# Kernel tuning notes

Hardware: AMD Instinct MI355X
Metric: run time of the kernel (lower is better)

Reference implementation:

```python
import jax, jax.numpy as jnp
import numpy as np

N = 100_000      # nodes
M = 200_000      # hyperedges
E = 1_000_000    # incidence pairs
D_IN = 64
HEADS, D_OUT = 8, 16   # linear out = 8*16 = 128


def setup_inputs() -> dict:
    key = jax.random.key(0)
    k = jax.random.split(key, 7)
    X = jax.random.normal(k[0], (N, D_IN), dtype=jnp.float32)
    vertex = jax.random.randint(k[1], (E,), 0, N, dtype=jnp.int32)
    edges = jax.random.randint(k[2], (E,), 0, M, dtype=jnp.int32)
    dege = jax.random.uniform(k[3], (M, 1), dtype=jnp.float32)
    degv = jax.random.uniform(k[4], (N, 1), dtype=jnp.float32)
    W = jax.random.normal(k[5], (D_IN, HEADS * D_OUT), dtype=jnp.float32) / np.sqrt(D_IN)
    b = jax.random.normal(k[6], (HEADS * D_OUT,), dtype=jnp.float32) * 0.01
    return {"X": X, "vertex": vertex, "edges": edges, "dege": dege, "degv": degv, "W": W, "b": b}


def reference(X, vertex, edges, dege, degv, W, b):
    n_nodes = X.shape[0]
    n_edges = dege.shape[0]
    # vertex -> hyperedge aggregation (first_aggregate = 'mean')
    Xve = X[vertex]                                               # [E, D]
    sums = jax.ops.segment_sum(Xve, edges, num_segments=n_edges)  # [M, D]
    counts = jax.ops.segment_sum(jnp.ones((edges.shape[0],), X.dtype), edges, num_segments=n_edges)
    Xe = sums / jnp.maximum(counts, 1.0)[:, None]                 # empty edges -> 0
    Xe = Xe * dege
    # hyperedge -> vertex aggregation (sum)
    Xev = Xe[edges]                                               # [E, D]
    Xv = jax.ops.segment_sum(Xev, vertex, num_segments=n_nodes)   # [N, D]
    Xv = Xv * degv
    # normalize_l2: row norm is computed on a DETACHED tensor in torch
    rownorm = jnp.linalg.norm(jax.lax.stop_gradient(Xv), axis=1, keepdims=True)
    scale = jnp.where(rownorm > 0, 1.0 / rownorm, 0.0)
    Xn = Xv * scale
    return Xn @ W + b
```

## Files before the change

kernel.cpp:

```cpp
#include <hip/hip_runtime.h>


#define DIN 64
#define DOUT 128
#define CH 4096
#define BSHIFT 9
#define FINE 512
#define PAYBITS 18
#define PAYMASK ((1u << PAYBITS) - 1u)
#define XB 256

typedef float f32x4 __attribute__((ext_vector_type(4)));
typedef short bf16x8 __attribute__((ext_vector_type(8)));

__device__ __forceinline__ unsigned short f2b(float f) {
  unsigned u = __float_as_uint(f);
  u = u + 0x7fffu + ((u >> 16) & 1u);
  return (unsigned short)(u >> 16);
}
__device__ __forceinline__ float b2f(unsigned s) {
  return __uint_as_float(s << 16);
}

__global__ __launch_bounds__(256) void k_p1(
    const int* __restrict__ vertex, const int* __restrict__ edges,
    int* __restrict__ G, const float* __restrict__ X,
    unsigned short* __restrict__ Xb, int* __restrict__ done,
    int E, int BKE, int BK, int NCH, int total4) {
  if (blockIdx.x == 0 && threadIdx.x == 0) *done = 0;
  if (blockIdx.x >= (unsigned)NCH) {
    int xb = blockIdx.x - NCH;
    for (int i = xb * 256 + threadIdx.x; i < total4; i += XB * 256) {
      float4 a = ((const float4*)X)[i];
      ushort4 r;
      r.x = f2b(a.x); r.y = f2b(a.y); r.z = f2b(a.z); r.w = f2b(a.w);
      ((ushort4*)Xb)[i] = r;
    }
    return;
  }
  __shared__ int h[1024];
  for (int i = threadIdx.x; i < BK; i += 256) h[i] = 0;
  __syncthreads();
  int c = blockIdx.x;
  int s = c * CH, e_ = min(E, s + CH);
  for (int i = s + threadIdx.x; i < e_; i += 256) {
    atomicAdd(&h[edges[i] >> BSHIFT], 1);
    atomicAdd(&h[BKE + (vertex[i] >> BSHIFT)], 1);
  }
  __syncthreads();
  for (int b = threadIdx.x; b < BK; b += 256) G[(size_t)b * NCH + c] = h[b];
}

__global__ __launch_bounds__(256) void k_p1b(
    int* __restrict__ G, int* __restrict__ rowTot, int* __restrict__ bucketBase,
    int* __restrict__ done, int NCH, int BK) {
  int b = blockIdx.x;
  int* row = G + (size_t)b * NCH;
  __shared__ int wsum[4];
  __shared__ int carry;
  __shared__ bool amLast;
  if (threadIdx.x == 0) carry = 0;
  __syncthreads();
  for (int base = 0; base < NCH; base += 256) {
    int i = base + threadIdx.x;
    int v = (i < NCH) ? row[i] : 0;
    int lane = threadIdx.x & 63, wid = threadIdx.x >> 6;
    int inc = v;
    #pragma unroll
    for (int o = 1; o < 64; o <<= 1) {
      int t = __shfl_up(inc, o);
      if (lane >= o) inc += t;
    }
    if (lane == 63) wsum[wid] = inc;
    __syncthreads();
    int woff = carry;
    for (int w = 0; w < wid; ++w) woff += wsum[w];
    int excl = woff + inc - v;
    if (i < NCH) row[i] = excl;
    __syncthreads();
    if (threadIdx.x == 0) carry += wsum[0] + wsum[1] + wsum[2] + wsum[3];
    __syncthreads();
  }
  if (threadIdx.x == 0) {
    rowTot[b] = carry;
    __threadfence();
    amLast = (atomicAdd(done, 1) == gridDim.x - 1);
  }
  __syncthreads();
  if (!amLast) return;

  if (threadIdx.x == 0) carry = 0;
  __syncthreads();
  for (int base = 0; base < BK; base += 256) {
    int i = base + threadIdx.x;
    int v = (i < BK) ? atomicAdd(&rowTot[i], 0) : 0;
    int lane = threadIdx.x & 63, wid = threadIdx.x >> 6;
    int inc = v;
    #pragma unroll
    for (int o = 1; o < 64; o <<= 1) {
      int t = __shfl_up(inc, o);
      if (lane >= o) inc += t;
    }
    if (lane == 63) wsum[wid] = inc;
    __syncthreads();
    int woff = carry;
    for (int w = 0; w < wid; ++w) woff += wsum[w];
    int excl = woff + inc - v;
    if (i < BK) bucketBase[i] = excl;
    __syncthreads();
    if (threadIdx.x == 0) carry += wsum[0] + wsum[1] + wsum[2] + wsum[3];
    __syncthreads();
  }
  if (threadIdx.x == 0) bucketBase[BK] = carry;
}

__global__ __launch_bounds__(256) void p2_scatter(
    const int* __restrict__ vertex, const int* __restrict__ edges,
    const int* __restrict__ G, const int* __restrict__ bucketBase,
    unsigned* __restrict__ temp, int E, int BKE, int BK, int NCH) {
  __shared__ int curs[1024];
  int c = blockIdx.x;
  for (int b = threadIdx.x; b < BK; b += 256)
    curs[b] = bucketBase[b] + G[(size_t)b * NCH + c];
  __syncthreads();
  int s = c * CH, e_ = min(E, s + CH);
  for (int i = s + threadIdx.x; i < e_; i += 256) {
    int e = edges[i], v = vertex[i];
    int pE = atomicAdd(&curs[e >> BSHIFT], 1);
    temp[pE] = ((unsigned)(e & (FINE - 1)) << PAYBITS) | (unsigned)v;
    int pV = atomicAdd(&curs[BKE + (v >> BSHIFT)], 1);
    temp[pV] = ((unsigned)(v & (FINE - 1)) << PAYBITS) | (unsigned)e;
  }
}

__global__ __launch_bounds__(256) void p3_sort(
    const unsigned* __restrict__ temp, const int* __restrict__ bucketBase,
    int* __restrict__ off, int* __restrict__ perm, int BKE, int M, int N) {
  __shared__ int hist[FINE];
  __shared__ int pos[FINE];
  __shared__ int wsum[4];
  int g = blockIdx.x;
  bool isE = g < BKE;
  int gg = isE ? g : g - BKE;
  int keyBase = gg << BSHIFT;
  int cap = isE ? M : N;
  int offBase = (isE ? 0 : M) + keyBase;
  int fineCount = min(FINE, cap - keyBase);
  int pairBase = bucketBase[g], pairEnd = bucketBase[g + 1];
  int cnt = pairEnd - pairBase;

  for (int i = threadIdx.x; i < FINE; i += 256) hist[i] = 0;
  __syncthreads();
  for (int i = threadIdx.x; i < cnt; i += 256)
    atomicAdd(&hist[temp[pairBase + i] >> PAYBITS], 1);
  __syncthreads();

  int t2 = threadIdx.x * 2;
  int a0 = hist[t2], a1 = hist[t2 + 1];
  int tsum = a0 + a1;
  int lane = threadIdx.x & 63, wid = threadIdx.x >> 6;
  int inc = tsum;
  #pragma unroll
  for (int o = 1; o < 64; o <<= 1) {
    int t = __shfl_up(inc, o);
    if (lane >= o) inc += t;
  }
  if (lane == 63) wsum[wid] = inc;
  __syncthreads();
  int woff = 0;
  for (int w = 0; w < wid; ++w) woff += wsum[w];
  int excl = woff + inc - tsum;
  pos[t2] = excl; pos[t2 + 1] = excl + a0;
  __syncthreads();

  for (int f = threadIdx.x; f < fineCount; f += 256)
    off[offBase + f] = pairBase + pos[f] + hist[f];
  for (int f = threadIdx.x; f < FINE; f += 256) pos[f] += pairBase;
  __syncthreads();

  for (int i = threadIdx.x; i < cnt; i += 256) {
    unsigned p = temp[pairBase + i];
    int q = atomicAdd(&pos[p >> PAYBITS], 1);
    perm[q] = (int)(p & PAYMASK);
  }
}


__global__ __launch_bounds__(256) void k_edge(
    const unsigned short* __restrict__ Xb, const int* __restrict__ off,
    const int* __restrict__ perm, const float* __restrict__ dege,
    unsigned short* __restrict__ Xe, int M) {
  long long gid = (long long)blockIdx.x * 256 + threadIdx.x;
  int wv = (int)(gid >> 6);
  int lane = threadIdx.x & 63;
  int g = lane >> 4, li = lane & 15;
  int e = wv * 4 + g;
  bool valid = e < M;
  int start = 0, end = 0;
  if (valid) { start = e ? off[e - 1] : 0; end = off[e]; }
  int deg = end - start;
  int myidx = (valid && li < deg) ? perm[start + li] : 0;
  int jmax = min(deg, 16);
  int jw = jmax;
  jw = max(jw, __shfl_xor(jw, 16));
  jw = max(jw, __shfl_xor(jw, 32));
  const uint2* X2 = (const uint2*)Xb;
  float4 acc = make_float4(0.f, 0.f, 0.f, 0.f);
  #pragma unroll 4
  for (int j = 0; j < jw; ++j) {
    int v0 = __shfl(myidx, (g << 4) + j);
    if (j < jmax) {
      uint2 a = X2[(size_t)v0 * 16 + li];
      acc.x += b2f(a.x & 0xffffu); acc.y += b2f(a.x >> 16);
      acc.z += b2f(a.y & 0xffffu); acc.w += b2f(a.y >> 16);
    }
  }
  for (int j = 16; j < deg; ++j) {
    int v0 = perm[start + j];
    uint2 a = X2[(size_t)v0 * 16 + li];
    acc.x += b2f(a.x & 0xffffu); acc.y += b2f(a.x >> 16);
    acc.z += b2f(a.y & 0xffffu); acc.w += b2f(a.y >> 16);
  }
  if (valid) {
    float s = dege[e] / fmaxf((float)deg, 1.0f);
    ushort4 r;
    r.x = f2b(acc.x * s); r.y = f2b(acc.y * s);
    r.z = f2b(acc.z * s); r.w = f2b(acc.w * s);
    ((ushort4*)Xe)[(size_t)e * 16 + li] = r;
  }
}

__global__ __launch_bounds__(256) void k_nodeagg(
    const unsigned short* __restrict__ Xe, const int* __restrict__ off,
    const int* __restrict__ perm, const float* __restrict__ degv,
    unsigned short* __restrict__ xn, int N, int M) {
  long long gid = (long long)blockIdx.x * 256 + threadIdx.x;
  int wv = (int)(gid >> 6);
  int lane = threadIdx.x & 63;
  int g = lane >> 4, li = lane & 15;
  int node = wv * 4 + g;
  bool valid = node < N;
  int start = 0, end = 0;
  if (valid) { start = off[M + node - 1]; end = off[M + node]; }
  int deg = end - start;
  int myidx = (valid && li < deg) ? perm[start + li] : 0;
  int jmax = min(deg, 16);
  int jw = jmax;
  jw = max(jw, __shfl_xor(jw, 16));
  jw = max(jw, __shfl_xor(jw, 32));
  const uint2* Xe2 = (const uint2*)Xe;
  float4 acc = make_float4(0.f, 0.f, 0.f, 0.f);
  #pragma unroll 4
  for (int j = 0; j < jw; ++j) {
    int e0 = __shfl(myidx, (g << 4) + j);
    if (j < jmax) {
      uint2 a = Xe2[(size_t)e0 * 16 + li];
      acc.x += b2f(a.x & 0xffffu); acc.y += b2f(a.x >> 16);
      acc.z += b2f(a.y & 0xffffu); acc.w += b2f(a.y >> 16);
    }
  }
  for (int j = 16; j < deg; ++j) {
    int e0 = perm[start + j];
    uint2 a = Xe2[(size_t)e0 * 16 + li];
    acc.x += b2f(a.x & 0xffffu); acc.y += b2f(a.x >> 16);
    acc.z += b2f(a.y & 0xffffu); acc.w += b2f(a.y >> 16);
  }
  float dv = valid ? degv[node] : 0.f;
  acc.x *= dv; acc.y *= dv; acc.z *= dv; acc.w *= dv;
  float ss = acc.x * acc.x + acc.y * acc.y + acc.z * acc.z + acc.w * acc.w;
  #pragma unroll
  for (int o = 1; o <= 8; o <<= 1) ss += __shfl_xor(ss, o);
  float sc = ss > 0.0f ? 1.0f / sqrtf(ss) : 0.0f;
  if (valid) {
    ushort4 r;
    r.x = f2b(acc.x * sc); r.y = f2b(acc.y * sc);
    r.z = f2b(acc.z * sc); r.w = f2b(acc.w * sc);
    ((ushort4*)xn)[(size_t)node * 16 + li] = r;
  }
}

#define WPAD 72
__global__ __launch_bounds__(256) void k_linear(
    const unsigned short* __restrict__ xn, const float* __restrict__ W,
    const float* __restrict__ bias, float* __restrict__ out, int N) {
  __shared__ unsigned short Wt[DOUT * WPAD];
  for (int i = threadIdx.x; i < DIN * DOUT; i += 256) {
    int k = i >> 7, c = i & 127;
    Wt[c * WPAD + k] = f2b(W[i]);
  }
  __syncthreads();
  int lane = threadIdx.x & 63;
  int wid = threadIdx.x >> 6;
  int r = lane & 15, h = lane >> 4;

  bf16x8 Bf[8][2];
  #pragma unroll
  for (int c = 0; c < 8; ++c) {
    #pragma unroll
    for (int ks = 0; ks < 2; ++ks) {
      int col = c * 16 + r;
      int k0 = ks * 32 + h * 8;
      Bf[c][ks] = *(const bf16x8*)&Wt[col * WPAD + k0];
    }
  }
  float bcol[8];
  #pragma unroll
  for (int c = 0; c < 8; ++c) bcol[c] = bias[c * 16 + r];

  int strips = (N + 15) >> 4;
  for (int s = blockIdx.x * 4 + wid; s < strips; s += gridDim.x * 4) {
    int row0 = s << 4;
    const unsigned short* xrow = xn + (size_t)(row0 + r) * DIN;
    bf16x8 a0 = *(const bf16x8*)&xrow[h * 8];
    bf16x8 a1 = *(const bf16x8*)&xrow[32 + h * 8];
    #pragma unroll
    for (int c = 0; c < 8; ++c) {
      f32x4 acc = {bcol[c], bcol[c], bcol[c], bcol[c]};
      acc = __builtin_amdgcn_mfma_f32_16x16x32_bf16(a0, Bf[c][0], acc, 0, 0, 0);
      acc = __builtin_amdgcn_mfma_f32_16x16x32_bf16(a1, Bf[c][1], acc, 0, 0, 0);
      #pragma unroll
      for (int q = 0; q < 4; ++q)
        out[(size_t)(row0 + h * 4 + q) * DOUT + c * 16 + r] = acc[q];
    }
  }
}

extern "C" void kernel_launch(void* const* d_in, const int* in_sizes, int n_in,
                              void* d_out, int out_size, void* d_ws, size_t ws_size,
                              hipStream_t stream) {
  const float* X      = (const float*)d_in[0];
  const int*   vertex = (const int*)d_in[1];
  const int*   edges  = (const int*)d_in[2];
  const float* dege   = (const float*)d_in[3];
  const float* degv   = (const float*)d_in[4];
  const float* W      = (const float*)d_in[5];
  const float* b      = (const float*)d_in[6];
  float* out = (float*)d_out;

  int N = in_sizes[0] / DIN;
  int E = in_sizes[1];
  int M = in_sizes[3];

  int NCH = (E + CH - 1) / CH;
  int BKE = (M + FINE - 1) >> BSHIFT;
  int BKV = (N + FINE - 1) >> BSHIFT;
  int BK  = BKE + BKV;

  unsigned short* Xe = (unsigned short*)d_ws;
  unsigned short* Xb = Xe + (size_t)M * DIN;
  int*   off  = (int*)(Xb + (size_t)N * DIN);
  int*   perm = off + (M + N);
  char*  R    = (char*)(perm + 2 * (size_t)E);
  unsigned*       temp = (unsigned*)R;
  unsigned short* xn   = (unsigned short*)R;
  size_t rBytes = (size_t)2 * E * 4;
  size_t xBytes = (size_t)N * DIN * 2;
  char*  R2   = R + (rBytes > xBytes ? rBytes : xBytes);
  int*   G    = (int*)R2;
  int*   rowTot = G + (size_t)BK * NCH;
  int*   bucketBase = rowTot + BK;
  int*   done = bucketBase + BK + 1;

  int total4 = N * DIN / 4;
  k_p1<<<NCH + XB, 256, 0, stream>>>(vertex, edges, G, X, Xb, done,
                                     E, BKE, BK, NCH, total4);
  k_p1b<<<BK, 256, 0, stream>>>(G, rowTot, bucketBase, done, NCH, BK);
  p2_scatter<<<NCH, 256, 0, stream>>>(vertex, edges, G, bucketBase, temp,
                                      E, BKE, BK, NCH);
  p3_sort<<<BK, 256, 0, stream>>>(temp, bucketBase, off, perm, BKE, M, N);

  int edgeBlocks = (M + 15) / 16;
  k_edge<<<edgeBlocks, 256, 0, stream>>>(Xb, off, perm, dege, Xe, M);

  int nodeBlocks = (N + 15) / 16;
  k_nodeagg<<<nodeBlocks, 256, 0, stream>>>(Xe, off, perm, degv, xn, N, M);

  int strips = (N + 15) >> 4;
  int linBlocks = (strips + 3) / 4;
  k_linear<<<linBlocks, 256, 0, stream>>>(xn, W, b, out, N);
}
```

Before: 147.4 us.

## Widen gather loads in edge kernel, process two nodes per lane group, vectorize histogram

```diff
diff --git a/kernel.cpp b/kernel.cpp
--- a/kernel.cpp
+++ b/kernel.cpp
@@ -43,7 +43,17 @@
   __syncthreads();
   int c = blockIdx.x;
   int s = c * CH, e_ = min(E, s + CH);
-  for (int i = s + threadIdx.x; i < e_; i += 256) {
+  int n4 = (e_ - s) >> 2;
+  const int4* ep = (const int4*)(edges + s);
+  const int4* vp = (const int4*)(vertex + s);
+  for (int i = threadIdx.x; i < n4; i += 256) {
+    int4 ee = ep[i], vv = vp[i];
+    atomicAdd(&h[ee.x >> BSHIFT], 1); atomicAdd(&h[ee.y >> BSHIFT], 1);
+    atomicAdd(&h[ee.z >> BSHIFT], 1); atomicAdd(&h[ee.w >> BSHIFT], 1);
+    atomicAdd(&h[BKE + (vv.x >> BSHIFT)], 1); atomicAdd(&h[BKE + (vv.y >> BSHIFT)], 1);
+    atomicAdd(&h[BKE + (vv.z >> BSHIFT)], 1); atomicAdd(&h[BKE + (vv.w >> BSHIFT)], 1);
+  }
+  for (int i = s + (n4 << 2) + threadIdx.x; i < e_; i += 256) {
     atomicAdd(&h[edges[i] >> BSHIFT], 1);
     atomicAdd(&h[BKE + (vertex[i] >> BSHIFT)], 1);
   }
@@ -193,40 +203,47 @@
   long long gid = (long long)blockIdx.x * 256 + threadIdx.x;
   int wv = (int)(gid >> 6);
   int lane = threadIdx.x & 63;
-  int g = lane >> 4, li = lane & 15;
-  int e = wv * 4 + g;
+  int g = lane >> 3, li = lane & 7;
+  int e = wv * 8 + g;
   bool valid = e < M;
   int start = 0, end = 0;
   if (valid) { start = e ? off[e - 1] : 0; end = off[e]; }
   int deg = end - start;
   int myidx = (valid && li < deg) ? perm[start + li] : 0;
-  int jmax = min(deg, 16);
+  int jmax = min(deg, 8);
   int jw = jmax;
+  jw = max(jw, __shfl_xor(jw, 8));
   jw = max(jw, __shfl_xor(jw, 16));
   jw = max(jw, __shfl_xor(jw, 32));
-  const uint2* X2 = (const uint2*)Xb;
-  float4 acc = make_float4(0.f, 0.f, 0.f, 0.f);
+  const uint4* X4 = (const uint4*)Xb;
+  float acc[8] = {0.f, 0.f, 0.f, 0.f, 0.f, 0.f, 0.f, 0.f};
   #pragma unroll 4
   for (int j = 0; j < jw; ++j) {
-    int v0 = __shfl(myidx, (g << 4) + j);
+    int v0 = __shfl(myidx, (g << 3) + j);
     if (j < jmax) {
-      uint2 a = X2[(size_t)v0 * 16 + li];
-      acc.x += b2f(a.x & 0xffffu); acc.y += b2f(a.x >> 16);
-      acc.z += b2f(a.y & 0xffffu); acc.w += b2f(a.y >> 16);
-    }
-  }
-  for (int j = 16; j < deg; ++j) {
+      uint4 a = X4[(size_t)v0 * 8 + li];
+      acc[0] += b2f(a.x & 0xffffu); acc[1] += b2f(a.x >> 16);
+      acc[2] += b2f(a.y & 0xffffu); acc[3] += b2f(a.y >> 16);
+      acc[4] += b2f(a.z & 0xffffu); acc[5] += b2f(a.z >> 16);
+      acc[6] += b2f(a.w & 0xffffu); acc[7] += b2f(a.w >> 16);
+    }
+  }
+  for (int j = 8; j < deg; ++j) {
     int v0 = perm[start + j];
-    uint2 a = X2[(size_t)v0 * 16 + li];
-    acc.x += b2f(a.x & 0xffffu); acc.y += b2f(a.x >> 16);
-    acc.z += b2f(a.y & 0xffffu); acc.w += b2f(a.y >> 16);
+    uint4 a = X4[(size_t)v0 * 8 + li];
+    acc[0] += b2f(a.x & 0xffffu); acc[1] += b2f(a.x >> 16);
+    acc[2] += b2f(a.y & 0xffffu); acc[3] += b2f(a.y >> 16);
+    acc[4] += b2f(a.z & 0xffffu); acc[5] += b2f(a.z >> 16);
+    acc[6] += b2f(a.w & 0xffffu); acc[7] += b2f(a.w >> 16);
   }
   if (valid) {
     float s = dege[e] / fmaxf((float)deg, 1.0f);
-    ushort4 r;
-    r.x = f2b(acc.x * s); r.y = f2b(acc.y * s);
-    r.z = f2b(acc.z * s); r.w = f2b(acc.w * s);
-    ((ushort4*)Xe)[(size_t)e * 16 + li] = r;
+    uint4 r;
+    r.x = (unsigned)f2b(acc[0] * s) | ((unsigned)f2b(acc[1] * s) << 16);
+    r.y = (unsigned)f2b(acc[2] * s) | ((unsigned)f2b(acc[3] * s) << 16);
+    r.z = (unsigned)f2b(acc[4] * s) | ((unsigned)f2b(acc[5] * s) << 16);
+    r.w = (unsigned)f2b(acc[6] * s) | ((unsigned)f2b(acc[7] * s) << 16);
+    ((uint4*)Xe)[(size_t)e * 8 + li] = r;
   }
 }
 
@@ -238,44 +255,74 @@
   int wv = (int)(gid >> 6);
   int lane = threadIdx.x & 63;
   int g = lane >> 4, li = lane & 15;
-  int node = wv * 4 + g;
-  bool valid = node < N;
-  int start = 0, end = 0;
-  if (valid) { start = off[M + node - 1]; end = off[M + node]; }
-  int deg = end - start;
-  int myidx = (valid && li < deg) ? perm[start + li] : 0;
-  int jmax = min(deg, 16);
-  int jw = jmax;
+  int base = wv * 8;
+  int nA = base + g;
+  int nB = base + 4 + g;
+  bool vA = nA < N, vB = nB < N;
+  int sA = 0, eA = 0, sB = 0, eB = 0;
+  if (vA) { sA = off[M + nA - 1]; eA = off[M + nA]; }
+  if (vB) { sB = off[M + nB - 1]; eB = off[M + nB]; }
+  int dA = eA - sA, dB = eB - sB;
+  int myA = (vA && li < dA) ? perm[sA + li] : 0;
+  int myB = (vB && li < dB) ? perm[sB + li] : 0;
+  int jA = min(dA, 16), jB = min(dB, 16);
+  int jw = max(jA, jB);
   jw = max(jw, __shfl_xor(jw, 16));
   jw = max(jw, __shfl_xor(jw, 32));
   const uint2* Xe2 = (const uint2*)Xe;
-  float4 acc = make_float4(0.f, 0.f, 0.f, 0.f);
-  #pragma unroll 4
+  float4 aA = make_float4(0.f, 0.f, 0.f, 0.f);
+  float4 aB = make_float4(0.f, 0.f, 0.f, 0.f);
+  #pragma unroll 2
   for (int j = 0; j < jw; ++j) {
-    int e0 = __shfl(myidx, (g << 4) + j);
-    if (j < jmax) {
-      uint2 a = Xe2[(size_t)e0 * 16 + li];
-      acc.x += b2f(a.x & 0xffffu); acc.y += b2f(a.x >> 16);
-      acc.z += b2f(a.y & 0xffffu); acc.w += b2f(a.y >> 16);
-    }
-  }
-  for (int j = 16; j < deg; ++j) {
-    int e0 = perm[start + j];
+    int iA = __shfl(myA, (g << 4) + j);
+    int iB = __shfl(myB, (g << 4) + j);
+    if (j < jA) {
+      uint2 a = Xe2[(size_t)iA * 16 + li];
+      aA.x += b2f(a.x & 0xffffu); aA.y += b2f(a.x >> 16);
+      aA.z += b2f(a.y & 0xffffu); aA.w += b2f(a.y >> 16);
+    }
+    if (j < jB) {
+      uint2 a = Xe2[(size_t)iB * 16 + li];
+      aB.x += b2f(a.x & 0xffffu); aB.y += b2f(a.x >> 16);
+      aB.z += b2f(a.y & 0xffffu); aB.w += b2f(a.y >> 16);
+    }
+  }
+  for (int j = 16; j < dA; ++j) {
+    int e0 = perm[sA + j];
     uint2 a = Xe2[(size_t)e0 * 16 + li];
-    acc.x += b2f(a.x & 0xffffu); acc.y += b2f(a.x >> 16);
-    acc.z += b2f(a.y & 0xffffu); acc.w += b2f(a.y >> 16);
-  }
-  float dv = valid ? degv[node] : 0.f;
-  acc.x *= dv; acc.y *= dv; acc.z *= dv; acc.w *= dv;
-  float ss = acc.x * acc.x + acc.y * acc.y + acc.z * acc.z + acc.w * acc.w;
+    aA.x += b2f(a.x & 0xffffu); aA.y += b2f(a.x >> 16);
+    aA.z += b2f(a.y & 0xffffu); aA.w += b2f(a.y >> 16);
+  }
+  for (int j = 16; j < dB; ++j) {
+    int e0 = perm[sB + j];
+    uint2 a = Xe2[(size_t)e0 * 16 + li];
+    aB.x += b2f(a.x & 0xffffu); aB.y += b2f(a.x >> 16);
+    aB.z += b2f(a.y & 0xffffu); aB.w += b2f(a.y >> 16);
+  }
+  float dvA = vA ? degv[nA] : 0.f;
+  float dvB = vB ? degv[nB] : 0.f;
+  aA.x *= dvA; aA.y *= dvA; aA.z *= dvA; aA.w *= dvA;
+  aB.x *= dvB; aB.y *= dvB; aB.z *= dvB; aB.w *= dvB;
+  float ssA = aA.x * aA.x + aA.y * aA.y + aA.z * aA.z + aA.w * aA.w;
+  float ssB = aB.x * aB.x + aB.y * aB.y + aB.z * aB.z + aB.w * aB.w;
   #pragma unroll
-  for (int o = 1; o <= 8; o <<= 1) ss += __shfl_xor(ss, o);
-  float sc = ss > 0.0f ? 1.0f / sqrtf(ss) : 0.0f;
-  if (valid) {
+  for (int o = 1; o <= 8; o <<= 1) {
+    ssA += __shfl_xor(ssA, o);
+    ssB += __shfl_xor(ssB, o);
+  }
+  float scA = ssA > 0.0f ? 1.0f / sqrtf(ssA) : 0.0f;
+  float scB = ssB > 0.0f ? 1.0f / sqrtf(ssB) : 0.0f;
+  if (vA) {
     ushort4 r;
-    r.x = f2b(acc.x * sc); r.y = f2b(acc.y * sc);
-    r.z = f2b(acc.z * sc); r.w = f2b(acc.w * sc);
-    ((ushort4*)xn)[(size_t)node * 16 + li] = r;
+    r.x = f2b(aA.x * scA); r.y = f2b(aA.y * scA);
+    r.z = f2b(aA.z * scA); r.w = f2b(aA.w * scA);
+    ((ushort4*)xn)[(size_t)nA * 16 + li] = r;
+  }
+  if (vB) {
+    ushort4 r;
+    r.x = f2b(aB.x * scB); r.y = f2b(aB.y * scB);
+    r.z = f2b(aB.z * scB); r.w = f2b(aB.w * scB);
+    ((ushort4*)xn)[(size_t)nB * 16 + li] = r;
   }
 }
 
@@ -369,10 +416,11 @@
                                       E, BKE, BK, NCH);
   p3_sort<<<BK, 256, 0, stream>>>(temp, bucketBase, off, perm, BKE, M, N);
 
-  int edgeBlocks = (M + 15) / 16;
+  int edgeBlocks = (M + 31) / 32;
   k_edge<<<edgeBlocks, 256, 0, stream>>>(Xb, off, perm, dege, Xe, M);
 
-  int nodeBlocks = (N + 15) / 16;
+  int nodeWaves = (N + 7) / 8;
+  int nodeBlocks = (nodeWaves + 3) / 4;
   k_nodeagg<<<nodeBlocks, 256, 0, stream>>>(Xe, off, perm, degv, xn, N, M);
 
   int strips = (N + 15) >> 4;
```

Result: faster. 135.7 us (-8.0%).
